# Kernel tuning notes

Measured on AMD Instinct MI355X. Metric: run time of the kernel, lower is better.

Reference implementation:

```python
import jax, jax.numpy as jnp
import numpy as np

N_NODE, N_REL = 200000, 64
DIM, N_FACTOR, N_LAYER, K, B = 64, 4, 2, 32, 1024


def setup_inputs() -> dict:
    key = jax.random.key(0)
    ks = jax.random.split(key, 12)
    node_emb = jax.random.normal(ks[0], (N_NODE, N_FACTOR, DIM), jnp.float32) * 0.05
    relation_emb = jax.random.normal(ks[1], (N_REL, N_FACTOR, DIM), jnp.float32) * 0.05
    # attention MLP: Linear(2d -> d), ReLU, Linear(d -> 1); stored as [in, out]
    W1 = jax.random.normal(ks[2], (2 * DIM, DIM), jnp.float32) * (1.0 / np.sqrt(2 * DIM))
    b1 = jnp.zeros((DIM,), jnp.float32)
    W2 = jax.random.normal(ks[3], (DIM, 1), jnp.float32) * (1.0 / np.sqrt(DIM))
    b2 = jnp.zeros((1,), jnp.float32)
    users = jax.random.randint(ks[4], (B,), 0, N_NODE)
    items = jax.random.randint(ks[5], (B,), 0, N_NODE)

    def make_triple(kh, kr, kt):
        h = jax.random.randint(kh, (B, 1, N_LAYER, K), 0, N_NODE)
        r = jax.random.randint(kr, (B, 1, N_LAYER, K), 0, N_REL)
        t = jax.random.randint(kt, (B, 1, N_LAYER, K), 0, N_NODE)
        return jnp.concatenate([h, r, t], axis=1)  # [B, 3, L, K]

    users_triple = make_triple(ks[6], ks[7], ks[8])
    items_triple = make_triple(ks[9], ks[10], ks[11])
    return {
        "node_emb": node_emb, "relation_emb": relation_emb,
        "W1": W1, "b1": b1, "W2": W2, "b2": b2,
        "users": users, "items": items,
        "users_triple": users_triple, "items_triple": items_triple,
    }


def _knowledge_attention(h_emb, t_emb, W1, b1, W2, b2):
    # h_emb, t_emb: [B, L, K, F, d]
    x = jnp.concatenate([h_emb, t_emb], axis=-1)          # [B,L,K,F,2d]
    hid = jax.nn.relu(x @ W1 + b1)                        # [B,L,K,F,d]
    logits = jnp.squeeze(hid @ W2 + b2, axis=-1)          # [B,L,K,F]
    w = jax.nn.softmax(logits, axis=2)                    # softmax over neighbors K
    return jnp.sum(w[..., None] * t_emb, axis=2)          # [B,L,F,d]


def _tower(node_emb, idx, triple, W1, b1, W2, b2):
    origin = node_emb[idx]                                # [B,F,d]
    h = node_emb[triple[:, 0]]                            # [B,L,K,F,d]
    t = node_emb[triple[:, 2]]                            # [B,L,K,F,d]
    layers = _knowledge_attention(h, t, W1, b1, W2, b2)   # [B,L,F,d]
    emb = jnp.concatenate([origin[:, None], layers], axis=1)  # [B,L+1,F,d]
    return jnp.transpose(emb, (1, 0, 2, 3))               # [L+1,B,F,d]


def reference(node_emb, relation_emb, W1, b1, W2, b2, users, items, users_triple, items_triple):
    # relation_emb is gathered in the original but never used by the attention math.
    u = _tower(node_emb, users, users_triple, W1, b1, W2, b2)
    v = _tower(node_emb, items, items_triple, W1, b1, W2, b2)
    return jnp.stack([u, v])  # [2, L+1, B, F, d]
```

## Files before the change

### kernel.cpp

```cpp
#include <hip/hip_runtime.h>
#include <hip/hip_bf16.h>
#include <math.h>

#define NNODE  200000
#define DIM    64
#define NF     4
#define NLAYER 2
#define KK     32
#define BB     1024

typedef __bf16 bf16x8 __attribute__((ext_vector_type(8)));
typedef __bf16 bf16x4 __attribute__((ext_vector_type(4)));
typedef float  f32x4  __attribute__((ext_vector_type(4)));

#define XSTRIDE 136

__global__ void prep_w1t(const float* __restrict__ W1, __bf16* __restrict__ w1t) {
    int j = blockIdx.x * 256 + threadIdx.x;
    int d = j >> 7, i = j & 127;
    w1t[j] = (__bf16)W1[i * 64 + d];
}

__global__ __launch_bounds__(256, 2) void kgat_mfma(
    const float* __restrict__ node_emb,
    const __bf16* __restrict__ w1t,
    const float* __restrict__ b1,
    const float* __restrict__ W2,
    const int*   __restrict__ users,
    const int*   __restrict__ items,
    const int*   __restrict__ users_triple,
    const int*   __restrict__ items_triple,
    float*       __restrict__ out)
{
    __shared__ __bf16 Xs[128 * XSTRIDE];
    __shared__ float  logitS[128];

    const int bid   = blockIdx.x;
    const int tower = bid >> 11;
    const int b     = (bid >> 1) & 1023;
    const int layer = bid & 1;
    const int tid   = threadIdx.x;
    const int w     = tid >> 6;
    const int lane  = tid & 63;
    const int m16   = lane & 15;
    const int quad  = lane >> 4;

    const int* __restrict__ triple = tower ? items_triple : users_triple;
    const int* __restrict__ idxarr = tower ? items : users;

    const int hbase = ((b * 3 + 0) * NLAYER + layer) * KK;
    const int tbase = ((b * 3 + 2) * NLAYER + layer) * KK;

    bf16x8 Bf[4][4];
#pragma unroll
    for (int nt = 0; nt < 4; ++nt)
#pragma unroll
        for (int kt = 0; kt < 4; ++kt)
            Bf[nt][kt] = *(const bf16x8*)(w1t + (nt * 16 + m16) * 128 + kt * 32 + quad * 8);

    {
        const int m = tid & 15;
#pragma unroll
        for (int r = 0; r < 4; ++r) {
            const int task = r * 16 + (tid >> 4);
            const int k    = task & 31;
            const int ch   = task >> 5;
            const int idx  = triple[(ch ? tbase : hbase) + k];
            const float* __restrict__ src = node_emb + (size_t)idx * (NF * DIM);
#pragma unroll
            for (int j = 0; j < 4; ++j) {
                f32x4 v = *(const f32x4*)(src + j * 64 + m * 4);
                bf16x4 bv;
#pragma unroll
                for (int u = 0; u < 4; ++u) bv[u] = (__bf16)v[u];
                *(bf16x4*)(&Xs[(j * 32 + k) * XSTRIDE + ch * 64 + m * 4]) = bv;
            }
        }
    }
    __syncthreads();

    f32x4 C[2][4];
#pragma unroll
    for (int mt = 0; mt < 2; ++mt)
#pragma unroll
        for (int nt = 0; nt < 4; ++nt) C[mt][nt] = (f32x4)(0.f);

    const __bf16* Arow0 = &Xs[(w * 32 + m16) * XSTRIDE];
    const __bf16* Arow1 = &Xs[(w * 32 + 16 + m16) * XSTRIDE];
#pragma unroll
    for (int kt = 0; kt < 4; ++kt) {
        bf16x8 A0 = *(const bf16x8*)(Arow0 + kt * 32 + quad * 8);
        bf16x8 A1 = *(const bf16x8*)(Arow1 + kt * 32 + quad * 8);
#pragma unroll
        for (int nt = 0; nt < 4; ++nt) {
            C[0][nt] = __builtin_amdgcn_mfma_f32_16x16x32_bf16(A0, Bf[nt][kt], C[0][nt], 0, 0, 0);
            C[1][nt] = __builtin_amdgcn_mfma_f32_16x16x32_bf16(A1, Bf[nt][kt], C[1][nt], 0, 0, 0);
        }
    }

    float b1v[4], w2v[4];
#pragma unroll
    for (int nt = 0; nt < 4; ++nt) {
        b1v[nt] = b1[nt * 16 + m16];
        w2v[nt] = W2[nt * 16 + m16];
    }
    float lsum[2][4];
#pragma unroll
    for (int mt = 0; mt < 2; ++mt)
#pragma unroll
        for (int r = 0; r < 4; ++r) {
            float s = 0.f;
#pragma unroll
            for (int nt = 0; nt < 4; ++nt)
                s += fmaxf(C[mt][nt][r] + b1v[nt], 0.f) * w2v[nt];
            lsum[mt][r] = s;
        }
#pragma unroll
    for (int off = 1; off < 16; off <<= 1)
#pragma unroll
        for (int mt = 0; mt < 2; ++mt)
#pragma unroll
            for (int r = 0; r < 4; ++r)
                lsum[mt][r] += __shfl_xor(lsum[mt][r], off, 64);

    if (m16 == 0) {
#pragma unroll
        for (int mt = 0; mt < 2; ++mt) {
            f32x4 v;
#pragma unroll
            for (int r = 0; r < 4; ++r) v[r] = lsum[mt][r];
            *(f32x4*)&logitS[w * 32 + mt * 16 + quad * 4] = v;
        }
    }
    __syncthreads();

    const float lg = logitS[w * 32 + (lane & 31)];
    float mx = lg;
#pragma unroll
    for (int off = 16; off; off >>= 1) mx = fmaxf(mx, __shfl_xor(mx, off, 64));
    const float e = __expf(lg - mx);
    float s = e;
#pragma unroll
    for (int off = 16; off; off >>= 1) s += __shfl_xor(s, off, 64);
    const float wgt = e / s;

    float oacc = 0.f;
#pragma unroll
    for (int k = 0; k < KK; ++k) {
        const float wk = __shfl(wgt, k, 64);
        oacc += wk * (float)Xs[(w * 32 + k) * XSTRIDE + 64 + lane];
    }
    out[(((size_t)(tower * 3 + 1 + layer) * BB + b) * NF + w) * DIM + lane] = oacc;

    if (layer == 0) {
        const int oid = idxarr[b];
        out[(((size_t)(tower * 3 + 0) * BB + b) * NF + w) * DIM + lane] =
            node_emb[((size_t)oid * NF + w) * DIM + lane];
    }
}

extern "C" void kernel_launch(void* const* d_in, const int* in_sizes, int n_in,
                              void* d_out, int out_size, void* d_ws, size_t ws_size,
                              hipStream_t stream) {
    const float* node_emb     = (const float*)d_in[0];
    const float* W1           = (const float*)d_in[2];
    const float* b1           = (const float*)d_in[3];
    const float* W2           = (const float*)d_in[4];
    const float* b2           = (const float*)d_in[5]; (void)b2;
    const int*   users        = (const int*)d_in[6];
    const int*   items        = (const int*)d_in[7];
    const int*   users_triple = (const int*)d_in[8];
    const int*   items_triple = (const int*)d_in[9];
    float* out = (float*)d_out;

    __bf16* w1t = (__bf16*)d_ws;

    hipLaunchKernelGGL(prep_w1t, dim3(32), dim3(256), 0, stream, W1, w1t);
    hipLaunchKernelGGL(kgat_mfma, dim3(2 * BB * NLAYER), dim3(256), 0, stream,
                       node_emb, w1t, b1, W2,
                       users, items, users_triple, items_triple, out);
}
```

Before: 304.0 us.

## Pre-convert node table to bf16 and gather half-width rows with skewed LDS

```diff
diff --git a/kernel.cpp b/kernel.cpp
--- a/kernel.cpp
+++ b/kernel.cpp
@@ -14,14 +14,28 @@
 typedef float  f32x4  __attribute__((ext_vector_type(4)));
 
 #define XSTRIDE 136
-
-__global__ void prep_w1t(const float* __restrict__ W1, __bf16* __restrict__ w1t) {
-    int j = blockIdx.x * 256 + threadIdx.x;
-    int d = j >> 7, i = j & 127;
-    w1t[j] = (__bf16)W1[i * 64 + d];
+#define FSKEW   8
+
+__global__ __launch_bounds__(256) void prep(
+    const float* __restrict__ ne, __bf16* __restrict__ nbf,
+    const float* __restrict__ W1, __bf16* __restrict__ w1t)
+{
+    const size_t t = (size_t)blockIdx.x * 256 + threadIdx.x;
+    const size_t i = t * 8;
+    f32x4 a = *(const f32x4*)(ne + i);
+    f32x4 b = *(const f32x4*)(ne + i + 4);
+    bf16x8 o;
+#pragma unroll
+    for (int u = 0; u < 4; ++u) { o[u] = (__bf16)a[u]; o[u + 4] = (__bf16)b[u]; }
+    *(bf16x8*)(nbf + i) = o;
+    if (t < 2 * DIM * DIM) {
+        const int d = (int)t >> 7, ii = (int)t & 127;
+        w1t[t] = (__bf16)W1[ii * DIM + d];
+    }
 }
 
-__global__ __launch_bounds__(256, 2) void kgat_mfma(
+__global__ __launch_bounds__(256, 4) void kgat_mfma(
+    const __bf16* __restrict__ nbf,
     const float* __restrict__ node_emb,
     const __bf16* __restrict__ w1t,
     const float* __restrict__ b1,
@@ -32,7 +46,7 @@
     const int*   __restrict__ items_triple,
     float*       __restrict__ out)
 {
-    __shared__ __bf16 Xs[128 * XSTRIDE];
+    __shared__ __bf16 Xs[128 * XSTRIDE + NF * FSKEW];
     __shared__ float  logitS[128];
 
     const int bid   = blockIdx.x;
@@ -51,6 +65,33 @@
     const int hbase = ((b * 3 + 0) * NLAYER + layer) * KK;
     const int tbase = ((b * 3 + 2) * NLAYER + layer) * KK;
 
+    {
+        const int m = tid & 15;
+        const int g = tid >> 4;
+        int kv[4], chv[4], idxv[4];
+#pragma unroll
+        for (int r = 0; r < 4; ++r) {
+            const int task = r * 16 + g;
+            kv[r]   = task & 31;
+            chv[r]  = task >> 5;
+            idxv[r] = triple[(chv[r] ? tbase : hbase) + kv[r]];
+        }
+        bf16x8 gv[4][2];
+#pragma unroll
+        for (int r = 0; r < 4; ++r) {
+            const __bf16* __restrict__ src = nbf + (size_t)idxv[r] * (NF * DIM) + m * 16;
+            gv[r][0] = *(const bf16x8*)(src);
+            gv[r][1] = *(const bf16x8*)(src + 8);
+        }
+        const int f = m >> 2, c = m & 3;
+#pragma unroll
+        for (int r = 0; r < 4; ++r) {
+            __bf16* dst = &Xs[(f * 32 + kv[r]) * XSTRIDE + f * FSKEW + chv[r] * 64 + c * 16];
+            *(bf16x8*)(dst)     = gv[r][0];
+            *(bf16x8*)(dst + 8) = gv[r][1];
+        }
+    }
+
     bf16x8 Bf[4][4];
 #pragma unroll
     for (int nt = 0; nt < 4; ++nt)
@@ -58,25 +99,6 @@
         for (int kt = 0; kt < 4; ++kt)
             Bf[nt][kt] = *(const bf16x8*)(w1t + (nt * 16 + m16) * 128 + kt * 32 + quad * 8);
 
-    {
-        const int m = tid & 15;
-#pragma unroll
-        for (int r = 0; r < 4; ++r) {
-            const int task = r * 16 + (tid >> 4);
-            const int k    = task & 31;
-            const int ch   = task >> 5;
-            const int idx  = triple[(ch ? tbase : hbase) + k];
-            const float* __restrict__ src = node_emb + (size_t)idx * (NF * DIM);
-#pragma unroll
-            for (int j = 0; j < 4; ++j) {
-                f32x4 v = *(const f32x4*)(src + j * 64 + m * 4);
-                bf16x4 bv;
-#pragma unroll
-                for (int u = 0; u < 4; ++u) bv[u] = (__bf16)v[u];
-                *(bf16x4*)(&Xs[(j * 32 + k) * XSTRIDE + ch * 64 + m * 4]) = bv;
-            }
-        }
-    }
     __syncthreads();
 
     f32x4 C[2][4];
@@ -85,8 +107,8 @@
 #pragma unroll
         for (int nt = 0; nt < 4; ++nt) C[mt][nt] = (f32x4)(0.f);
 
-    const __bf16* Arow0 = &Xs[(w * 32 + m16) * XSTRIDE];
-    const __bf16* Arow1 = &Xs[(w * 32 + 16 + m16) * XSTRIDE];
+    const __bf16* Arow0 = &Xs[(w * 32 + m16) * XSTRIDE + w * FSKEW];
+    const __bf16* Arow1 = &Xs[(w * 32 + 16 + m16) * XSTRIDE + w * FSKEW];
 #pragma unroll
     for (int kt = 0; kt < 4; ++kt) {
         bf16x8 A0 = *(const bf16x8*)(Arow0 + kt * 32 + quad * 8);
@@ -148,7 +170,7 @@
 #pragma unroll
     for (int k = 0; k < KK; ++k) {
         const float wk = __shfl(wgt, k, 64);
-        oacc += wk * (float)Xs[(w * 32 + k) * XSTRIDE + 64 + lane];
+        oacc += wk * (float)Xs[(w * 32 + k) * XSTRIDE + w * FSKEW + 64 + lane];
     }
     out[(((size_t)(tower * 3 + 1 + layer) * BB + b) * NF + w) * DIM + lane] = oacc;
 
@@ -174,9 +196,11 @@
     float* out = (float*)d_out;
 
     __bf16* w1t = (__bf16*)d_ws;
-
-    hipLaunchKernelGGL(prep_w1t, dim3(32), dim3(256), 0, stream, W1, w1t);
+    __bf16* nbf = (__bf16*)((char*)d_ws + 16384);
+
+    hipLaunchKernelGGL(prep, dim3(NNODE * NF * DIM / 8 / 256), dim3(256), 0, stream,
+                       node_emb, nbf, W1, w1t);
     hipLaunchKernelGGL(kgat_mfma, dim3(2 * BB * NLAYER), dim3(256), 0, stream,
-                       node_emb, w1t, b1, W2,
+                       nbf, node_emb, w1t, b1, W2,
                        users, items, users_triple, items_triple, out);
 }
```

Measured after the change: 347.8 us. 1.14x slower.
